# Optimization experiments

Hardware: AMD Instinct MI355X
Metric: run time of the kernel (lower is better)

## Reference

```python
import jax, jax.numpy as jnp
import numpy as np

EMBED_DIM = 1024
NUM_HEADS = 16
HEAD_DIM = EMBED_DIM // NUM_HEADS


def setup_inputs() -> dict:
    key = jax.random.key(0)
    k1, k2, k3, k4, k5 = jax.random.split(key, 5)
    s = 1.0 / np.sqrt(EMBED_DIM)
    return {
        "query": jax.random.normal(k1, (8, 1024, EMBED_DIM), dtype=jnp.float32),
        "w_qkv": jax.random.normal(k2, (EMBED_DIM, 3 * EMBED_DIM), dtype=jnp.float32) * s,
        "b_qkv": jax.random.normal(k3, (3 * EMBED_DIM,), dtype=jnp.float32) * 0.01,
        "w_proj": jax.random.normal(k4, (EMBED_DIM, EMBED_DIM), dtype=jnp.float32) * s,
        "b_proj": jax.random.normal(k5, (EMBED_DIM,), dtype=jnp.float32) * 0.01,
    }


def reference(query, w_qkv, b_qkv, w_proj, b_proj):
    B, S, D = query.shape
    H, Hd = NUM_HEADS, HEAD_DIM
    scale = 1.0 / jnp.sqrt(jnp.asarray(Hd, query.dtype))
    # fused QKV projection; key=value=query (self-attention), so one GEMM suffices
    qkv = query @ w_qkv + b_qkv                      # [B, S, 3D]
    qkv = qkv.reshape(B, S, 3, H, Hd)
    q = qkv[:, :, 0].transpose(0, 2, 1, 3)           # [B, H, S, Hd]
    k = qkv[:, :, 1].transpose(0, 2, 1, 3)
    v = qkv[:, :, 2].transpose(0, 2, 1, 3)
    attn = jnp.einsum("bhqd,bhkd->bhqk", q, k) * scale
    attn = jax.nn.softmax(attn, axis=-1)
    out = jnp.einsum("bhqk,bhkd->bhqd", attn, v)     # [B, H, S, Hd]
    out = out.transpose(0, 2, 1, 3).reshape(B, S, D)
    return out @ w_proj + b_proj
```

## Files before the change

### kernel.cpp

```cpp
#include <hip/hip_runtime.h>
#include <stdint.h>

#define DEV __device__ __forceinline__

typedef short bf16x8 __attribute__((ext_vector_type(8)));
typedef float f32x4 __attribute__((ext_vector_type(4)));
typedef float f32x16 __attribute__((ext_vector_type(16)));
typedef unsigned u32x2 __attribute__((ext_vector_type(2)));

DEV short f2bf(float f) {
  uint32_t x = __builtin_bit_cast(uint32_t, f);
  uint32_t r = x + 0x7fffu + ((x >> 16) & 1u);
  return (short)(r >> 16);
}

DEV unsigned cvtpk(float lo, float hi) {
  unsigned r;
  asm("v_cvt_pk_bf16_f32 %0, %1, %2" : "=v"(r) : "v"(lo), "v"(hi));
  return r;
}
DEV void pswap(unsigned& a, unsigned& b) {
  asm("v_permlane32_swap_b32 %0, %1" : "+v"(a), "+v"(b));
}

DEV void gld16(const short* g, short* l) {
  __builtin_amdgcn_global_load_lds(
      (const __attribute__((address_space(1))) void*)g,
      (__attribute__((address_space(3))) void*)l, 16, 0, 0);
}

__global__ __launch_bounds__(256) void k_cvt(const float* __restrict__ in,
                                             short* __restrict__ out, int n8) {
  int i = blockIdx.x * 256 + threadIdx.x;
  if (i >= n8) return;
  const float4* p = (const float4*)in + (size_t)i * 2;
  float4 a = p[0], b = p[1];
  bf16x8 v;
  v[0] = f2bf(a.x); v[1] = f2bf(a.y); v[2] = f2bf(a.z); v[3] = f2bf(a.w);
  v[4] = f2bf(b.x); v[5] = f2bf(b.y); v[6] = f2bf(b.z); v[7] = f2bf(b.w);
  *(bf16x8*)(out + (size_t)i * 8) = v;
}

__global__ __launch_bounds__(256) void k_tcvt(const float* __restrict__ in,
                                              short* __restrict__ out, int K, int N) {
  __shared__ float tile[64][65];
  int t = threadIdx.x;
  int n0 = blockIdx.x * 64, k0 = blockIdx.y * 64;
  int kl = t >> 4, nl = (t & 15) * 4;
#pragma unroll
  for (int it = 0; it < 4; ++it) {
    float4 v = *(const float4*)&in[(size_t)(k0 + kl + it * 16) * N + n0 + nl];
    tile[nl + 0][kl + it * 16] = v.x;
    tile[nl + 1][kl + it * 16] = v.y;
    tile[nl + 2][kl + it * 16] = v.z;
    tile[nl + 3][kl + it * 16] = v.w;
  }
  __syncthreads();
  int no = t >> 2, kc = (t & 3) * 16;
  bf16x8 v0, v1;
#pragma unroll
  for (int c = 0; c < 8; ++c) v0[c] = f2bf(tile[no][kc + c]);
#pragma unroll
  for (int c = 0; c < 8; ++c) v1[c] = f2bf(tile[no][kc + 8 + c]);
  size_t ob = (size_t)(n0 + no) * K + k0 + kc;
  *(bf16x8*)&out[ob] = v0;
  *(bf16x8*)&out[ob + 8] = v1;
}

__global__ __launch_bounds__(256) void k_vt(const short* __restrict__ vin,
                                            short* __restrict__ vt) {
  __shared__ alignas(16) short tile[64][72];
  int t = threadIdx.x;
  int sc = blockIdx.x, bh = blockIdx.y;
  int sl = t >> 3, dc = (t & 7) * 8;
  const short* base = vin + ((size_t)bh * 1024 + sc * 64) * 64;
#pragma unroll
  for (int it = 0; it < 2; ++it)
    *(bf16x8*)&tile[sl + it * 32][dc] = *(const bf16x8*)&base[(size_t)(sl + it * 32) * 64 + dc];
  __syncthreads();
  int d = t >> 2, s2 = (t & 3) * 16;
  bf16x8 v0, v1;
#pragma unroll
  for (int c = 0; c < 8; ++c) v0[c] = tile[s2 + c][d];
#pragma unroll
  for (int c = 0; c < 8; ++c) v1[c] = tile[s2 + 8 + c][d];
  size_t ob = (size_t)bh * 65536 + (size_t)d * 1024 + sc * 64 + s2;
  *(bf16x8*)&vt[ob] = v0;
  *(bf16x8*)&vt[ob + 8] = v1;
}

template <int MODE>
__global__ __launch_bounds__(256) void k_gemm(const short* __restrict__ A,
                                              const short* __restrict__ Bw,
                                              const float* __restrict__ bias,
                                              void* o0, void* o1, void* o2) {
  __shared__ alignas(16) short lA[128 * 64];
  __shared__ alignas(16) short lB[128 * 64];
  int t = threadIdx.x;
  int w = t >> 6, l = t & 63;
  int wr = w >> 1, wc = w & 1;
  int lr = l & 15, lg = l >> 4;
  int m0 = blockIdx.y * 128, n0 = blockIdx.x * 128;
  f32x4 acc[4][4] = {};

  int srow = t >> 3;
  int schunk = (t & 7) ^ (srow & 7);
  const short* ap = A + (size_t)(m0 + srow) * 1024 + schunk * 8;
  const short* bp = Bw + (size_t)(n0 + srow) * 1024 + schunk * 8;
  short* la0 = &lA[(size_t)w * 8 * 64];
  short* lb0 = &lB[(size_t)w * 8 * 64];

  for (int k0 = 0; k0 < 1024; k0 += 64) {
#pragma unroll
    for (int c = 0; c < 4; ++c) {
      gld16(ap + (size_t)c * 32 * 1024 + k0, la0 + c * 32 * 64);
      gld16(bp + (size_t)c * 32 * 1024 + k0, lb0 + c * 32 * 64);
    }
    __syncthreads();
    bf16x8 af[4][2], bfr[4][2];
#pragma unroll
    for (int i = 0; i < 4; ++i)
#pragma unroll
      for (int kh = 0; kh < 2; ++kh) {
        int ra = wr * 64 + i * 16 + lr;
        int rb = wc * 64 + i * 16 + lr;
        af[i][kh] = *(const bf16x8*)&lA[ra * 64 + (((kh * 4 + lg) ^ (ra & 7)) * 8)];
        bfr[i][kh] = *(const bf16x8*)&lB[rb * 64 + (((kh * 4 + lg) ^ (rb & 7)) * 8)];
      }
#pragma unroll
    for (int i = 0; i < 4; ++i)
#pragma unroll
      for (int j = 0; j < 4; ++j)
#pragma unroll
        for (int kh = 0; kh < 2; ++kh)
          acc[i][j] = __builtin_amdgcn_mfma_f32_16x16x32_bf16(af[i][kh], bfr[j][kh], acc[i][j], 0, 0, 0);
    __syncthreads();
  }

  if (MODE == 0) {
    short* outs[3] = {(short*)o0, (short*)o1, (short*)o2};
    short* op = outs[n0 >> 10];
    float qs = (n0 < 1024) ? 0.18033688011112042f : 1.0f;
#pragma unroll
    for (int i = 0; i < 4; ++i)
#pragma unroll
      for (int j = 0; j < 4; ++j)
#pragma unroll
        for (int r = 0; r < 4; ++r) {
          int mm = m0 + wr * 64 + i * 16 + lg * 4 + r;
          int nn = n0 + wc * 64 + j * 16 + lr;
          float val = (acc[i][j][r] + bias[nn]) * qs;
          int hh = (nn >> 6) & 15, dd = nn & 63;
          int bb = mm >> 10, ss = mm & 1023;
          op[((size_t)(bb * 16 + hh) * 1024 + ss) * 64 + dd] = f2bf(val);
        }
  } else {
    float* op = (float*)o0;
#pragma unroll
    for (int i = 0; i < 4; ++i)
#pragma unroll
      for (int j = 0; j < 4; ++j)
#pragma unroll
        for (int r = 0; r < 4; ++r) {
          int mm = m0 + wr * 64 + i * 16 + lg * 4 + r;
          int nn = n0 + wc * 64 + j * 16 + lr;
          op[(size_t)mm * 1024 + nn] = acc[i][j][r] + bias[nn];
        }
  }
}

__global__ __launch_bounds__(256, 4) void k_attn(const short* __restrict__ qb,
                                                 const short* __restrict__ kb,
                                                 const short* __restrict__ vt,
                                                 short* __restrict__ ao) {
  __shared__ alignas(16) short lds[2 * 8192];
  int t = threadIdx.x, w = t >> 6, l = t & 63;
  int r0 = l & 31, hi = l >> 5;

  int bid = blockIdx.x;
  int swz = (bid & 7) * 128 + (bid >> 3);
  int bh = swz >> 3, qc = swz & 7;
  int q0 = qc * 128 + w * 32;

  const short* qbase = qb + (size_t)bh * 65536;
  const short* kbase = kb + (size_t)bh * 65536;
  const short* vbase = vt + (size_t)bh * 65536;

  bf16x8 qf[4];
#pragma unroll
  for (int step = 0; step < 4; ++step)
    qf[step] = *(const bf16x8*)&qbase[(size_t)(q0 + r0) * 64 + step * 16 + hi * 8];

  f32x16 acc0 = {0,0,0,0,0,0,0,0,0,0,0,0,0,0,0,0};
  f32x16 acc1 = {0,0,0,0,0,0,0,0,0,0,0,0,0,0,0,0};
  float ls = 0.f;

  int srow = t >> 3;
  int sch = (t & 7) ^ (srow & 7);
  const short* kp = kbase + (size_t)srow * 64 + sch * 8;
  const short* vp = vbase + (size_t)srow * 1024 + sch * 8;

#define STAGE(buf, kv0)                                              \
  do {                                                               \
    short* dk = &lds[(buf) * 8192 + w * 512];                        \
    short* dv = &lds[(buf) * 8192 + 4096 + w * 512];                 \
    gld16(kp + (size_t)(kv0) * 64, dk);                              \
    gld16(kp + (size_t)((kv0) + 32) * 64, dk + 2048);                \
    gld16(vp + (kv0), dv);                                           \
    gld16(vp + (kv0) + 32 * 1024, dv + 2048);                        \
  } while (0)

  STAGE(0, 0);
  int cur = 0;
  for (int it = 0; it < 16; ++it) {
    __syncthreads();
    if (it < 15) STAGE(cur ^ 1, (it + 1) * 64);
    const short* lk = &lds[cur * 8192];
    const short* lv = &lds[cur * 8192 + 4096];

    f32x16 s0 = {0,0,0,0,0,0,0,0,0,0,0,0,0,0,0,0};
    f32x16 s1 = {0,0,0,0,0,0,0,0,0,0,0,0,0,0,0,0};
    __builtin_amdgcn_s_setprio(1);
#pragma unroll
    for (int step = 0; step < 4; ++step) {
      int ck = step * 2 + hi;
      bf16x8 kf0 = *(const bf16x8*)&lk[r0 * 64 + ((ck ^ (r0 & 7)) * 8)];
      int r1 = 32 + r0;
      bf16x8 kf1 = *(const bf16x8*)&lk[r1 * 64 + ((ck ^ (r1 & 7)) * 8)];
      s0 = __builtin_amdgcn_mfma_f32_32x32x16_bf16(kf0, qf[step], s0, 0, 0, 0);
      s1 = __builtin_amdgcn_mfma_f32_32x32x16_bf16(kf1, qf[step], s1, 0, 0, 0);
    }
    __builtin_amdgcn_s_setprio(0);

    float rs = 0.f;
#pragma unroll
    for (int r = 0; r < 16; ++r) { float p = __builtin_exp2f(s0[r]); s0[r] = p; rs += p; }
#pragma unroll
    for (int r = 0; r < 16; ++r) { float p = __builtin_exp2f(s1[r]); s1[r] = p; rs += p; }
    rs += __shfl_xor(rs, 32);
    ls += rs;

    __builtin_amdgcn_s_setprio(1);
#pragma unroll
    for (int tt = 0; tt < 2; ++tt) {
#pragma unroll
      for (int ks = 0; ks < 2; ++ks) {
        unsigned Aw, Bw2, Cw, Dw;
        if (tt == 0) {
          Aw = cvtpk(s0[8 * ks + 0], s0[8 * ks + 1]);
          Bw2 = cvtpk(s0[8 * ks + 4], s0[8 * ks + 5]);
          Cw = cvtpk(s0[8 * ks + 2], s0[8 * ks + 3]);
          Dw = cvtpk(s0[8 * ks + 6], s0[8 * ks + 7]);
        } else {
          Aw = cvtpk(s1[8 * ks + 0], s1[8 * ks + 1]);
          Bw2 = cvtpk(s1[8 * ks + 4], s1[8 * ks + 5]);
          Cw = cvtpk(s1[8 * ks + 2], s1[8 * ks + 3]);
          Dw = cvtpk(s1[8 * ks + 6], s1[8 * ks + 7]);
        }
        pswap(Aw, Bw2);
        pswap(Cw, Dw);
        union { unsigned u[4]; bf16x8 v; } pb;
        pb.u[0] = Aw; pb.u[1] = Cw; pb.u[2] = Bw2; pb.u[3] = Dw;
        int cv = tt * 4 + ks * 2 + hi;
        bf16x8 vf0 = *(const bf16x8*)&lv[r0 * 64 + ((cv ^ (r0 & 7)) * 8)];
        int r1 = 32 + r0;
        bf16x8 vf1 = *(const bf16x8*)&lv[r1 * 64 + ((cv ^ (r1 & 7)) * 8)];
        acc0 = __builtin_amdgcn_mfma_f32_32x32x16_bf16(vf0, pb.v, acc0, 0, 0, 0);
        acc1 = __builtin_amdgcn_mfma_f32_32x32x16_bf16(vf1, pb.v, acc1, 0, 0, 0);
      }
    }
    __builtin_amdgcn_s_setprio(0);
    cur ^= 1;
  }
#undef STAGE

  __syncthreads();
  short* ep = &lds[w * 2048];
  float inv = 1.0f / ls;
#pragma unroll
  for (int d0 = 0; d0 < 2; ++d0) {
#pragma unroll
    for (int q4 = 0; q4 < 4; ++q4) {
      unsigned w0, w1;
      if (d0 == 0) {
        w0 = cvtpk(acc0[q4 * 4 + 0] * inv, acc0[q4 * 4 + 1] * inv);
        w1 = cvtpk(acc0[q4 * 4 + 2] * inv, acc0[q4 * 4 + 3] * inv);
      } else {
        w0 = cvtpk(acc1[q4 * 4 + 0] * inv, acc1[q4 * 4 + 1] * inv);
        w1 = cvtpk(acc1[q4 * 4 + 2] * inv, acc1[q4 * 4 + 3] * inv);
      }
      int chunk = (q4 + 4 * d0) ^ (r0 & 7);
      u32x2 uv; uv[0] = w0; uv[1] = w1;
      *(u32x2*)((char*)ep + r0 * 128 + chunk * 16 + hi * 8) = uv;
    }
  }
  int b = bh >> 4, hh = bh & 15;
#pragma unroll
  for (int rr = 0; rr < 4; ++rr) {
    int row = (l >> 3) + rr * 8;
    int c = (l & 7) ^ (row & 7);
    bf16x8 ov = *(const bf16x8*)((char*)ep + row * 128 + c * 16);
    int tok = b * 1024 + q0 + row;
    *(bf16x8*)&ao[(size_t)tok * 1024 + hh * 64 + (l & 7) * 8] = ov;
  }
}

extern "C" void kernel_launch(void* const* d_in, const int* in_sizes, int n_in,
                              void* d_out, int out_size, void* d_ws, size_t ws_size,
                              hipStream_t stream) {
  const float* query  = (const float*)d_in[0];
  const float* w_qkv  = (const float*)d_in[1];
  const float* b_qkv  = (const float*)d_in[2];
  const float* w_proj = (const float*)d_in[3];
  const float* b_proj = (const float*)d_in[4];
  float* out = (float*)d_out;
  char* ws = (char*)d_ws;

  short* qbf = (short*)(ws);
  short* wT  = (short*)(ws + 16777216);
  short* wpT = (short*)(ws + 23068672);
  short* qb  = (short*)(ws + 25165824);
  short* kb  = (short*)(ws + 41943040);
  short* vb  = (short*)(ws + 58720256);
  short* vt  = (short*)(ws + 75497472);
  short* ao  = qbf;

  k_cvt<<<4096, 256, 0, stream>>>(query, qbf, 1048576);
  k_tcvt<<<dim3(48, 16), 256, 0, stream>>>(w_qkv, wT, 1024, 3072);
  k_tcvt<<<dim3(16, 16), 256, 0, stream>>>(w_proj, wpT, 1024, 1024);
  k_gemm<0><<<dim3(24, 64), 256, 0, stream>>>(qbf, wT, b_qkv, qb, kb, vb);
  k_vt<<<dim3(16, 128), 256, 0, stream>>>(vb, vt);
  k_attn<<<1024, 256, 0, stream>>>(qb, kb, vt, ao);
  k_gemm<1><<<dim3(8, 64), 256, 0, stream>>>(ao, wpT, b_proj, out, nullptr, nullptr);
}
```

Baseline: 179.1 us.

## Double-buffer GEMM LDS tiles to overlap global loads with MFMA

```diff
diff --git a/kernel.cpp b/kernel.cpp
--- a/kernel.cpp
+++ b/kernel.cpp
@@ -94,8 +94,8 @@
                                               const short* __restrict__ Bw,
                                               const float* __restrict__ bias,
                                               void* o0, void* o1, void* o2) {
-  __shared__ alignas(16) short lA[128 * 64];
-  __shared__ alignas(16) short lB[128 * 64];
+  __shared__ alignas(16) short lA[2][128 * 64];
+  __shared__ alignas(16) short lB[2][128 * 64];
   int t = threadIdx.x;
   int w = t >> 6, l = t & 63;
   int wr = w >> 1, wc = w & 1;
@@ -107,16 +107,32 @@
   int schunk = (t & 7) ^ (srow & 7);
   const short* ap = A + (size_t)(m0 + srow) * 1024 + schunk * 8;
   const short* bp = Bw + (size_t)(n0 + srow) * 1024 + schunk * 8;
-  short* la0 = &lA[(size_t)w * 8 * 64];
-  short* lb0 = &lB[(size_t)w * 8 * 64];
-
-  for (int k0 = 0; k0 < 1024; k0 += 64) {
-#pragma unroll
-    for (int c = 0; c < 4; ++c) {
-      gld16(ap + (size_t)c * 32 * 1024 + k0, la0 + c * 32 * 64);
-      gld16(bp + (size_t)c * 32 * 1024 + k0, lb0 + c * 32 * 64);
+  int lofs = w * 8 * 64;
+
+#define GSTAGE(buf, k0)                                                  \
+  do {                                                                   \
+    short* la0 = &lA[buf][lofs];                                         \
+    short* lb0 = &lB[buf][lofs];                                         \
+    _Pragma("unroll")                                                    \
+    for (int c = 0; c < 4; ++c) {                                        \
+      gld16(ap + (size_t)c * 32 * 1024 + (k0), la0 + c * 32 * 64);       \
+      gld16(bp + (size_t)c * 32 * 1024 + (k0), lb0 + c * 32 * 64);       \
+    }                                                                    \
+  } while (0)
+
+  GSTAGE(0, 0);
+  for (int it = 0; it < 16; ++it) {
+    int p = it & 1;
+    if (it < 15) {
+      GSTAGE(p ^ 1, (it + 1) * 64);
+      asm volatile("s_waitcnt vmcnt(8)" ::: "memory");
+    } else {
+      asm volatile("s_waitcnt vmcnt(0)" ::: "memory");
     }
-    __syncthreads();
+    __builtin_amdgcn_sched_barrier(0);
+    __builtin_amdgcn_s_barrier();
+    __builtin_amdgcn_sched_barrier(0);
+
     bf16x8 af[4][2], bfr[4][2];
 #pragma unroll
     for (int i = 0; i < 4; ++i)
@@ -124,9 +140,10 @@
       for (int kh = 0; kh < 2; ++kh) {
         int ra = wr * 64 + i * 16 + lr;
         int rb = wc * 64 + i * 16 + lr;
-        af[i][kh] = *(const bf16x8*)&lA[ra * 64 + (((kh * 4 + lg) ^ (ra & 7)) * 8)];
-        bfr[i][kh] = *(const bf16x8*)&lB[rb * 64 + (((kh * 4 + lg) ^ (rb & 7)) * 8)];
+        af[i][kh] = *(const bf16x8*)&lA[p][ra * 64 + (((kh * 4 + lg) ^ (ra & 7)) * 8)];
+        bfr[i][kh] = *(const bf16x8*)&lB[p][rb * 64 + (((kh * 4 + lg) ^ (rb & 7)) * 8)];
       }
+    __builtin_amdgcn_s_setprio(1);
 #pragma unroll
     for (int i = 0; i < 4; ++i)
 #pragma unroll
@@ -134,8 +151,13 @@
 #pragma unroll
         for (int kh = 0; kh < 2; ++kh)
           acc[i][j] = __builtin_amdgcn_mfma_f32_16x16x32_bf16(af[i][kh], bfr[j][kh], acc[i][j], 0, 0, 0);
-    __syncthreads();
-  }
+    __builtin_amdgcn_s_setprio(0);
+
+    __builtin_amdgcn_sched_barrier(0);
+    __builtin_amdgcn_s_barrier();
+    __builtin_amdgcn_sched_barrier(0);
+  }
+#undef GSTAGE
 
   if (MODE == 0) {
     short* outs[3] = {(short*)o0, (short*)o1, (short*)o2};
```

After: 183.3 us. 2.4% more time.
